# Kernel tuning notes

Hardware: AMD Instinct MI355X
Metric: run time of the kernel (lower is better)

## Reference

```python
import jax, jax.numpy as jnp
import numpy as np

B = 4096
MAX_ATOMS = 2048


def setup_inputs() -> dict:
    key = jax.random.key(0)
    k1, k2, k3 = jax.random.split(key, 3)
    coords_input = jax.random.normal(k1, (B, 3 * MAX_ATOMS), dtype=jnp.float32) * 10.0
    coords_target = jax.random.normal(k2, (B, 3 * MAX_ATOMS), dtype=jnp.float32) * 10.0
    num_atoms = jax.random.randint(k3, (B,), 64, MAX_ATOMS + 1, dtype=jnp.int32)
    return {"coords_input": coords_input, "coords_target": coords_target, "num_atoms": num_atoms}


def _kabsch_rmsd(coords_input, coords_target, num_atoms):
    b, f = coords_input.shape
    n_max = f // 3
    x = coords_input.reshape(b, n_max, 3)   # [B, N, 3] interleaved xyz per atom
    y = coords_target.reshape(b, n_max, 3)
    mask = (jnp.arange(n_max)[None, :] < num_atoms[:, None])[..., None]  # [B, N, 1]
    n = num_atoms.astype(x.dtype)[:, None, None]                          # [B, 1, 1]

    # masked centroids, then center and zero out padded atoms
    xm = jnp.where(mask, x, 0.0)
    ym = jnp.where(mask, y, 0.0)
    xc = (x - xm.sum(axis=1, keepdims=True) / n) * mask
    yc = (y - ym.sum(axis=1, keepdims=True) / n) * mask

    # 3x3 cross-covariance per batch element
    C = jnp.einsum('bni,bnj->bij', xc, yc)  # [B, 3, 3]
    s = jnp.linalg.svd(C, compute_uv=False)  # singular values, descending [B, 3]
    # Kabsch determinant correction: d = sign(det(U) det(V)) = sign(det(C))
    d = jnp.where(jnp.linalg.det(C) < 0.0, -1.0, 1.0).astype(x.dtype)
    trace = s[:, 0] + s[:, 1] + d * s[:, 2]

    gx = jnp.sum(xc * xc, axis=(1, 2))
    gy = jnp.sum(yc * yc, axis=(1, 2))
    msd = (gx + gy - 2.0 * trace) / jnp.squeeze(n, (1, 2))
    return jnp.sqrt(jnp.maximum(msd, 0.0))


def reference(coords_input, coords_target, num_atoms):
    return _kabsch_rmsd(coords_input, coords_target, num_atoms)
```

## Files before the change

kernel.cpp:

```cpp
#include <hip/hip_runtime.h>
#include <math.h>

#define NBLK 256
#define N_MAX 2048

#define ACC_ATOM(X0,X1,X2,Y0,Y1,Y2,M) do {                          \
    const float m_ = (M);                                           \
    const float x0 = (X0)*m_, x1 = (X1)*m_, x2 = (X2)*m_;           \
    const float y0 = (Y0)*m_, y1 = (Y1)*m_, y2 = (Y2)*m_;           \
    acc[0]  += x0;    acc[1]  += x1;    acc[2]  += x2;              \
    acc[3]  += y0;    acc[4]  += y1;    acc[5]  += y2;              \
    acc[6]  += x0*y0; acc[7]  += x0*y1; acc[8]  += x0*y2;           \
    acc[9]  += x1*y0; acc[10] += x1*y1; acc[11] += x1*y2;           \
    acc[12] += x2*y0; acc[13] += x2*y1; acc[14] += x2*y2;           \
    acc[15] += x0*x0 + x1*x1 + x2*x2;                               \
    acc[16] += y0*y0 + y1*y1 + y2*y2;                               \
} while (0)

__global__ __launch_bounds__(NBLK) void kabsch_rmsd_kernel(
    const float* __restrict__ X, const float* __restrict__ Y,
    const int* __restrict__ num_atoms, float* __restrict__ out)
{
    const int b = blockIdx.x;
    const int t = threadIdx.x;
    const int n = num_atoms[b];

    const float4* __restrict__ x4 =
        reinterpret_cast<const float4*>(X + (size_t)b * (3 * N_MAX));
    const float4* __restrict__ y4 =
        reinterpret_cast<const float4*>(Y + (size_t)b * (3 * N_MAX));

    float acc[17];
#pragma unroll
    for (int i = 0; i < 17; ++i) acc[i] = 0.0f;

    for (int a0 = 4 * t; a0 < n; a0 += 4 * NBLK) {
        const int fi = 3 * (a0 >> 2);
        const float4 xa = x4[fi + 0], xb = x4[fi + 1], xc = x4[fi + 2];
        const float4 ya = y4[fi + 0], yb = y4[fi + 1], yc = y4[fi + 2];
        const float m1 = (a0 + 1 < n) ? 1.0f : 0.0f;
        const float m2 = (a0 + 2 < n) ? 1.0f : 0.0f;
        const float m3 = (a0 + 3 < n) ? 1.0f : 0.0f;
        ACC_ATOM(xa.x, xa.y, xa.z, ya.x, ya.y, ya.z, 1.0f);
        ACC_ATOM(xa.w, xb.x, xb.y, ya.w, yb.x, yb.y, m1);
        ACC_ATOM(xb.z, xb.w, xc.x, yb.z, yb.w, yc.x, m2);
        ACC_ATOM(xc.y, xc.z, xc.w, yc.y, yc.z, yc.w, m3);
    }

#pragma unroll
    for (int i = 0; i < 17; ++i) {
#pragma unroll
        for (int off = 32; off > 0; off >>= 1)
            acc[i] += __shfl_down(acc[i], off);
    }

    __shared__ float lds[17 * 4];
    const int wave = t >> 6;
    const int lane = t & 63;
    if (lane == 0) {
#pragma unroll
        for (int i = 0; i < 17; ++i) lds[i * 4 + wave] = acc[i];
    }
    __syncthreads();

    if (t == 0) {
        double s[17];
#pragma unroll
        for (int i = 0; i < 17; ++i)
            s[i] = (double)lds[i * 4 + 0] + (double)lds[i * 4 + 1] +
                   (double)lds[i * 4 + 2] + (double)lds[i * 4 + 3];

        const double dn = (double)n;
        const double Sx0 = s[0], Sx1 = s[1], Sx2 = s[2];
        const double Sy0 = s[3], Sy1 = s[4], Sy2 = s[5];

        double C[3][3];
        C[0][0] = s[6]  - Sx0 * Sy0 / dn;
        C[0][1] = s[7]  - Sx0 * Sy1 / dn;
        C[0][2] = s[8]  - Sx0 * Sy2 / dn;
        C[1][0] = s[9]  - Sx1 * Sy0 / dn;
        C[1][1] = s[10] - Sx1 * Sy1 / dn;
        C[1][2] = s[11] - Sx1 * Sy2 / dn;
        C[2][0] = s[12] - Sx2 * Sy0 / dn;
        C[2][1] = s[13] - Sx2 * Sy1 / dn;
        C[2][2] = s[14] - Sx2 * Sy2 / dn;

        const double gx = s[15] - (Sx0*Sx0 + Sx1*Sx1 + Sx2*Sx2) / dn;
        const double gy = s[16] - (Sy0*Sy0 + Sy1*Sy1 + Sy2*Sy2) / dn;

        const double det =
            C[0][0] * (C[1][1]*C[2][2] - C[1][2]*C[2][1]) -
            C[0][1] * (C[1][0]*C[2][2] - C[1][2]*C[2][0]) +
            C[0][2] * (C[1][0]*C[2][1] - C[1][1]*C[2][0]);

        double A00 = C[0][0]*C[0][0] + C[1][0]*C[1][0] + C[2][0]*C[2][0];
        double A11 = C[0][1]*C[0][1] + C[1][1]*C[1][1] + C[2][1]*C[2][1];
        double A22 = C[0][2]*C[0][2] + C[1][2]*C[1][2] + C[2][2]*C[2][2];
        double A01 = C[0][0]*C[0][1] + C[1][0]*C[1][1] + C[2][0]*C[2][1];
        double A02 = C[0][0]*C[0][2] + C[1][0]*C[1][2] + C[2][0]*C[2][2];
        double A12 = C[0][1]*C[0][2] + C[1][1]*C[1][2] + C[2][1]*C[2][2];

        double e0, e1, e2;
        const double q  = (A00 + A11 + A22) / 3.0;
        const double p1 = A01*A01 + A02*A02 + A12*A12;
        const double p2 = (A00-q)*(A00-q) + (A11-q)*(A11-q) + (A22-q)*(A22-q)
                          + 2.0 * p1;
        if (p2 <= 0.0) {
            e0 = e1 = e2 = q;
        } else {
            const double p = sqrt(p2 / 6.0);
            const double ip = 1.0 / p;
            const double b00 = (A00 - q) * ip, b11 = (A11 - q) * ip,
                         b22 = (A22 - q) * ip;
            const double b01 = A01 * ip, b02 = A02 * ip, b12 = A12 * ip;
            double r = 0.5 * (b00 * (b11*b22 - b12*b12)
                            - b01 * (b01*b22 - b12*b02)
                            + b02 * (b01*b12 - b11*b02));
            r = fmin(1.0, fmax(-1.0, r));
            const double phi = acos(r) / 3.0;
            e0 = q + 2.0 * p * cos(phi);
            e2 = q + 2.0 * p * cos(phi + 2.0943951023931953);
            e1 = 3.0 * q - e0 - e2;
        }

        const double s0 = sqrt(fmax(e0, 0.0));
        const double s1 = sqrt(fmax(e1, 0.0));
        const double s2 = sqrt(fmax(e2, 0.0));
        const double dsign = (det < 0.0) ? -1.0 : 1.0;
        const double trace = s0 + s1 + dsign * s2;

        const double msd = (gx + gy - 2.0 * trace) / dn;
        out[b] = (float)sqrt(fmax(msd, 0.0));
    }
}

extern "C" void kernel_launch(void* const* d_in, const int* in_sizes, int n_in,
                              void* d_out, int out_size, void* d_ws, size_t ws_size,
                              hipStream_t stream) {
    const float* coords_input  = (const float*)d_in[0];
    const float* coords_target = (const float*)d_in[1];
    const int*   num_atoms     = (const int*)d_in[2];
    float* out = (float*)d_out;

    const int B = out_size;
    kabsch_rmsd_kernel<<<B, NBLK, 0, stream>>>(coords_input, coords_target,
                                               num_atoms, out);
}
```

Before: 198.0 us.

## Split per-molecule reduction across two waves and move epilogue to separate kernel

Replaces the one-block-per-molecule design with two independent 64-lane waves per molecule that each accumulate half of the atoms and write 17 partial sums to workspace. A second kernel then combines the partials and runs the double-precision 3x3 eigen/SVD epilogue with one thread per molecule. This removes the LDS reduction and barrier and the serial single-thread epilogue tail inside the bandwidth-bound block, and balances the work better for variable atom counts. In exchange it adds a second launch and a workspace round-trip, and each wave must keep more loads in flight.

Result: no change. 200.6 us (+1.3%).

```diff
diff --git a/kernel.cpp b/kernel.cpp
--- a/kernel.cpp
+++ b/kernel.cpp
@@ -1,8 +1,8 @@
 #include <hip/hip_runtime.h>
 #include <math.h>
 
-#define NBLK 256
 #define N_MAX 2048
+#define HALVES 2
 
 #define ACC_ATOM(X0,X1,X2,Y0,Y1,Y2,M) do {                          \
     const float m_ = (M);                                           \
@@ -17,13 +17,19 @@
     acc[16] += y0*y0 + y1*y1 + y2*y2;                               \
 } while (0)
 
-__global__ __launch_bounds__(NBLK) void kabsch_rmsd_kernel(
+__global__ __launch_bounds__(256) void kabsch_sums_kernel(
     const float* __restrict__ X, const float* __restrict__ Y,
-    const int* __restrict__ num_atoms, float* __restrict__ out)
+    const int* __restrict__ num_atoms, float* __restrict__ ws, int B)
 {
-    const int b = blockIdx.x;
-    const int t = threadIdx.x;
-    const int n = num_atoms[b];
+    const int wave = threadIdx.x >> 6;
+    const int lane = threadIdx.x & 63;
+    const int gw   = blockIdx.x * 4 + wave;
+    const int b    = gw / HALVES;
+    const int h    = gw % HALVES;
+    if (b >= B) return;
+
+    const int n  = num_atoms[b];
+    const int nq = (n + 3) >> 2;
 
     const float4* __restrict__ x4 =
         reinterpret_cast<const float4*>(X + (size_t)b * (3 * N_MAX));
@@ -34,8 +40,9 @@
 #pragma unroll
     for (int i = 0; i < 17; ++i) acc[i] = 0.0f;
 
-    for (int a0 = 4 * t; a0 < n; a0 += 4 * NBLK) {
-        const int fi = 3 * (a0 >> 2);
+    for (int q = h * 64 + lane; q < nq; q += 64 * HALVES) {
+        const int a0 = 4 * q;
+        const int fi = 3 * q;
         const float4 xa = x4[fi + 0], xb = x4[fi + 1], xc = x4[fi + 2];
         const float4 ya = y4[fi + 0], yb = y4[fi + 1], yc = y4[fi + 2];
         const float m1 = (a0 + 1 < n) ? 1.0f : 0.0f;
@@ -54,84 +61,91 @@
             acc[i] += __shfl_down(acc[i], off);
     }
 
-    __shared__ float lds[17 * 4];
-    const int wave = t >> 6;
-    const int lane = t & 63;
     if (lane == 0) {
 #pragma unroll
-        for (int i = 0; i < 17; ++i) lds[i * 4 + wave] = acc[i];
+        for (int i = 0; i < 17; ++i)
+            ws[(size_t)(h * 17 + i) * B + b] = acc[i];
     }
-    __syncthreads();
+}
 
-    if (t == 0) {
-        double s[17];
+__global__ __launch_bounds__(256) void kabsch_epilogue_kernel(
+    const float* __restrict__ ws, const int* __restrict__ num_atoms,
+    float* __restrict__ out, int B)
+{
+    const int b = blockIdx.x * 256 + threadIdx.x;
+    if (b >= B) return;
+
+    double s[17];
 #pragma unroll
-        for (int i = 0; i < 17; ++i)
-            s[i] = (double)lds[i * 4 + 0] + (double)lds[i * 4 + 1] +
-                   (double)lds[i * 4 + 2] + (double)lds[i * 4 + 3];
+    for (int i = 0; i < 17; ++i) {
+        double v = 0.0;
+#pragma unroll
+        for (int h = 0; h < HALVES; ++h)
+            v += (double)ws[(size_t)(h * 17 + i) * B + b];
+        s[i] = v;
+    }
 
-        const double dn = (double)n;
-        const double Sx0 = s[0], Sx1 = s[1], Sx2 = s[2];
-        const double Sy0 = s[3], Sy1 = s[4], Sy2 = s[5];
+    const double dn = (double)num_atoms[b];
+    const double Sx0 = s[0], Sx1 = s[1], Sx2 = s[2];
+    const double Sy0 = s[3], Sy1 = s[4], Sy2 = s[5];
 
-        double C[3][3];
-        C[0][0] = s[6]  - Sx0 * Sy0 / dn;
-        C[0][1] = s[7]  - Sx0 * Sy1 / dn;
-        C[0][2] = s[8]  - Sx0 * Sy2 / dn;
-        C[1][0] = s[9]  - Sx1 * Sy0 / dn;
-        C[1][1] = s[10] - Sx1 * Sy1 / dn;
-        C[1][2] = s[11] - Sx1 * Sy2 / dn;
-        C[2][0] = s[12] - Sx2 * Sy0 / dn;
-        C[2][1] = s[13] - Sx2 * Sy1 / dn;
-        C[2][2] = s[14] - Sx2 * Sy2 / dn;
+    double C[3][3];
+    C[0][0] = s[6]  - Sx0 * Sy0 / dn;
+    C[0][1] = s[7]  - Sx0 * Sy1 / dn;
+    C[0][2] = s[8]  - Sx0 * Sy2 / dn;
+    C[1][0] = s[9]  - Sx1 * Sy0 / dn;
+    C[1][1] = s[10] - Sx1 * Sy1 / dn;
+    C[1][2] = s[11] - Sx1 * Sy2 / dn;
+    C[2][0] = s[12] - Sx2 * Sy0 / dn;
+    C[2][1] = s[13] - Sx2 * Sy1 / dn;
+    C[2][2] = s[14] - Sx2 * Sy2 / dn;
 
-        const double gx = s[15] - (Sx0*Sx0 + Sx1*Sx1 + Sx2*Sx2) / dn;
-        const double gy = s[16] - (Sy0*Sy0 + Sy1*Sy1 + Sy2*Sy2) / dn;
+    const double gx = s[15] - (Sx0*Sx0 + Sx1*Sx1 + Sx2*Sx2) / dn;
+    const double gy = s[16] - (Sy0*Sy0 + Sy1*Sy1 + Sy2*Sy2) / dn;
 
-        const double det =
-            C[0][0] * (C[1][1]*C[2][2] - C[1][2]*C[2][1]) -
-            C[0][1] * (C[1][0]*C[2][2] - C[1][2]*C[2][0]) +
-            C[0][2] * (C[1][0]*C[2][1] - C[1][1]*C[2][0]);
+    const double det =
+        C[0][0] * (C[1][1]*C[2][2] - C[1][2]*C[2][1]) -
+        C[0][1] * (C[1][0]*C[2][2] - C[1][2]*C[2][0]) +
+        C[0][2] * (C[1][0]*C[2][1] - C[1][1]*C[2][0]);
 
-        double A00 = C[0][0]*C[0][0] + C[1][0]*C[1][0] + C[2][0]*C[2][0];
-        double A11 = C[0][1]*C[0][1] + C[1][1]*C[1][1] + C[2][1]*C[2][1];
-        double A22 = C[0][2]*C[0][2] + C[1][2]*C[1][2] + C[2][2]*C[2][2];
-        double A01 = C[0][0]*C[0][1] + C[1][0]*C[1][1] + C[2][0]*C[2][1];
-        double A02 = C[0][0]*C[0][2] + C[1][0]*C[1][2] + C[2][0]*C[2][2];
-        double A12 = C[0][1]*C[0][2] + C[1][1]*C[1][2] + C[2][1]*C[2][2];
+    double A00 = C[0][0]*C[0][0] + C[1][0]*C[1][0] + C[2][0]*C[2][0];
+    double A11 = C[0][1]*C[0][1] + C[1][1]*C[1][1] + C[2][1]*C[2][1];
+    double A22 = C[0][2]*C[0][2] + C[1][2]*C[1][2] + C[2][2]*C[2][2];
+    double A01 = C[0][0]*C[0][1] + C[1][0]*C[1][1] + C[2][0]*C[2][1];
+    double A02 = C[0][0]*C[0][2] + C[1][0]*C[1][2] + C[2][0]*C[2][2];
+    double A12 = C[0][1]*C[0][2] + C[1][1]*C[1][2] + C[2][1]*C[2][2];
 
-        double e0, e1, e2;
-        const double q  = (A00 + A11 + A22) / 3.0;
-        const double p1 = A01*A01 + A02*A02 + A12*A12;
-        const double p2 = (A00-q)*(A00-q) + (A11-q)*(A11-q) + (A22-q)*(A22-q)
-                          + 2.0 * p1;
-        if (p2 <= 0.0) {
-            e0 = e1 = e2 = q;
-        } else {
-            const double p = sqrt(p2 / 6.0);
-            const double ip = 1.0 / p;
-            const double b00 = (A00 - q) * ip, b11 = (A11 - q) * ip,
-                         b22 = (A22 - q) * ip;
-            const double b01 = A01 * ip, b02 = A02 * ip, b12 = A12 * ip;
-            double r = 0.5 * (b00 * (b11*b22 - b12*b12)
-                            - b01 * (b01*b22 - b12*b02)
-                            + b02 * (b01*b12 - b11*b02));
-            r = fmin(1.0, fmax(-1.0, r));
-            const double phi = acos(r) / 3.0;
-            e0 = q + 2.0 * p * cos(phi);
-            e2 = q + 2.0 * p * cos(phi + 2.0943951023931953);
-            e1 = 3.0 * q - e0 - e2;
-        }
+    double e0, e1, e2;
+    const double q  = (A00 + A11 + A22) / 3.0;
+    const double p1 = A01*A01 + A02*A02 + A12*A12;
+    const double p2 = (A00-q)*(A00-q) + (A11-q)*(A11-q) + (A22-q)*(A22-q)
+                      + 2.0 * p1;
+    if (p2 <= 0.0) {
+        e0 = e1 = e2 = q;
+    } else {
+        const double p = sqrt(p2 / 6.0);
+        const double ip = 1.0 / p;
+        const double b00 = (A00 - q) * ip, b11 = (A11 - q) * ip,
+                     b22 = (A22 - q) * ip;
+        const double b01 = A01 * ip, b02 = A02 * ip, b12 = A12 * ip;
+        double r = 0.5 * (b00 * (b11*b22 - b12*b12)
+                        - b01 * (b01*b22 - b12*b02)
+                        + b02 * (b01*b12 - b11*b02));
+        r = fmin(1.0, fmax(-1.0, r));
+        const double phi = acos(r) / 3.0;
+        e0 = q + 2.0 * p * cos(phi);
+        e2 = q + 2.0 * p * cos(phi + 2.0943951023931953);
+        e1 = 3.0 * q - e0 - e2;
+    }
 
-        const double s0 = sqrt(fmax(e0, 0.0));
-        const double s1 = sqrt(fmax(e1, 0.0));
-        const double s2 = sqrt(fmax(e2, 0.0));
-        const double dsign = (det < 0.0) ? -1.0 : 1.0;
-        const double trace = s0 + s1 + dsign * s2;
+    const double s0 = sqrt(fmax(e0, 0.0));
+    const double s1 = sqrt(fmax(e1, 0.0));
+    const double s2 = sqrt(fmax(e2, 0.0));
+    const double dsign = (det < 0.0) ? -1.0 : 1.0;
+    const double trace = s0 + s1 + dsign * s2;
 
-        const double msd = (gx + gy - 2.0 * trace) / dn;
-        out[b] = (float)sqrt(fmax(msd, 0.0));
-    }
+    const double msd = (gx + gy - 2.0 * trace) / dn;
+    out[b] = (float)sqrt(fmax(msd, 0.0));
 }
 
 extern "C" void kernel_launch(void* const* d_in, const int* in_sizes, int n_in,
@@ -141,8 +155,13 @@
     const float* coords_target = (const float*)d_in[1];
     const int*   num_atoms     = (const int*)d_in[2];
     float* out = (float*)d_out;
+    float* ws  = (float*)d_ws;
 
     const int B = out_size;
-    kabsch_rmsd_kernel<<<B, NBLK, 0, stream>>>(coords_input, coords_target,
-                                               num_atoms, out);
+    const int waves = B * HALVES;
+    const int blocksA = (waves + 3) / 4;
+    kabsch_sums_kernel<<<blocksA, 256, 0, stream>>>(coords_input, coords_target,
+                                                    num_atoms, ws, B);
+    const int blocksB = (B + 255) / 256;
+    kabsch_epilogue_kernel<<<blocksB, 256, 0, stream>>>(ws, num_atoms, out, B);
 }
```
